# Kernel tuning notes

Hardware: AMD Instinct MI355X
Metric: run time of the kernel (lower is better)

The kernel has to match this reference:

```python
import jax, jax.numpy as jnp
import numpy as np

KS = 5
NF = 64
B, H, W = 2, 160, 160


def _conv1x1(x, w, b):
    # x: (B,Ci,H,W), w: (Co,Ci)
    return jnp.einsum('oi,bihw->bohw', w, x) + b[None, :, None, None]


def _conv2x2(x, w, b, dil):
    # x: (B,1,Hp,Wp), w: (64,1,2,2); VALID conv with dilation dil
    y = jax.lax.conv_general_dilated(x, w, (1, 1), 'VALID',
                                     rhs_dilation=(dil, dil),
                                     dimension_numbers=('NCHW', 'OIHW', 'NCHW'))
    return y + b[None, :, None, None]


def _conv_s(x, w, b):
    # conv1 module, mode 's': gather taps (0,0),(1,1),(1,2),(2,1) of each 3x3 patch,
    # then (1,4) conv == linear combo of 4 shifted images.
    h = x.shape[2] - 2
    wd = x.shape[3] - 2
    x0 = x[:, 0]
    taps = jnp.stack([x0[:, 0:h, 0:wd],
                      x0[:, 1:h + 1, 1:wd + 1],
                      x0[:, 1:h + 1, 2:wd + 2],
                      x0[:, 2:h + 2, 1:wd + 1]], axis=1)  # (B,4,h,wd)
    return jnp.einsum('ok,bkhw->bohw', w.reshape(NF, 4), taps) + b[None, :, None, None]


def _construct(c, dense_ps):
    # relu then dense 1x1-conv chain with channel concat, final 1x1 -> 4 channels
    x = jax.nn.relu(c)
    for (wt, bs) in dense_ps[:-1]:
        feat = jax.nn.relu(_conv1x1(x, wt, bs))
        x = jnp.concatenate([x, feat], axis=1)
    wt, bs = dense_ps[-1]
    return _conv1x1(x, wt, bs)


def _ag(x, sigx, sigy, theta, sigr):
    # x: (B,ks,ks,HW); params: (B,HW). Per-pixel anisotropic bilateral kernel.
    ks = x.shape[1]
    r = jnp.arange(ks, dtype=x.dtype) - ks // 2
    sq = (r[:, None] ** 2 + r[None, :] ** 2)[None, :, :, None]  # (1,ks,ks,1)
    sx = sigx[:, None, None, :]
    sy = sigy[:, None, None, :]
    th = theta[:, None, None, :]
    sr = sigr[:, None, None, :]
    spatial = jnp.exp(-sq / (2.0 * sr ** 2))
    disx = jnp.abs(x[:, ks // 2:ks // 2 + 1] - x)       # center row
    disy = jnp.abs(x[:, :, ks // 2:ks // 2 + 1] - x)    # center col
    a = sx * disx
    bb = sy * disy
    color = jnp.exp(-0.5 * (a ** 2 - 2.0 * th * a * bb + bb ** 2))
    kern = spatial * color
    kern = kern / jnp.sum(kern, axis=(1, 2), keepdims=True)
    return jnp.sum(kern * x, axis=(1, 2))  # (B,HW)


def _forward(x_in, conv1x_w, conv1x_b, conv1c_w, conv1c_b, conv1cs_w, conv1cs_b,
             w2, b2, w3, b3, w4, b4, w5, b5, w6, b6):
    dense_ps = [(w2, b2), (w3, b3), (w4, b4), (w5, b5), (w6, b6)]

    def fk(x, mod):
        if mod == 's':
            c = _conv_s(x, conv1cs_w, conv1cs_b)
        elif mod == 'c':
            c = _conv2x2(x, conv1c_w, conv1c_b, 2)
        else:
            c = _conv2x2(x, conv1x_w, conv1x_b, 1)
        return _construct(c, dense_ps)

    def mode_ens(x, p, mod):
        pad = lambda z: jnp.pad(z, ((0, 0), (0, 0), (0, p), (0, p)), mode='reflect')
        r0 = fk(pad(x), mod)
        r2 = jnp.rot90(fk(pad(jnp.rot90(x, 2, (2, 3))), mod), 2, (2, 3))
        r1 = jnp.rot90(fk(pad(jnp.rot90(x, 1, (2, 3))), mod), 3, (2, 3))
        r3 = jnp.rot90(fk(pad(jnp.rot90(x, 3, (2, 3))), mod), 1, (2, 3))
        return (r0 + r2) / 2.0, (r1 + r3) / 2.0

    e1x, e2x = mode_ens(x_in, 1, 'x')
    e1s, e2s = mode_ens(x_in, 2, 's')
    e1c, e2c = mode_ens(x_in, 2, 'c')
    par = (e1x + e2x + e1s + e2s + e1c + e2c) / 6.0  # (B,4,H,W)

    b, c, h, w = x_in.shape
    sigx = jnp.clip(jax.nn.sigmoid(par[:, 0]).reshape(b, -1) + 1e-6, 0.0, 1.0)
    sigy = jnp.clip(jax.nn.sigmoid(par[:, 1]).reshape(b, -1) + 1e-6, 0.0, 1.0)
    theta = jnp.clip(jnp.tanh(par[:, 2]).reshape(b, -1), -1.0, 1.0)
    sigr = jnp.clip(jnp.tanh(par[:, 3]).reshape(b, -1) + 1e-6, -1.0, 1.0)

    ph = KS // 2
    xt = jnp.pad(x_in, ((0, 0), (0, 0), (ph, ph), (ph, ph)))  # zero pad
    # unfold -> (B, KS, KS, H*W)
    patches = jnp.stack([jnp.stack([xt[:, 0, i:i + h, j:j + w].reshape(b, -1)
                                    for j in range(KS)], axis=1)
                         for i in range(KS)], axis=1)
    outs = _ag(patches, sigx * 20.0, sigy * 20.0, theta, sigr * 10.0 + 10.0).reshape(b, c, h, w)
    return outs, sigx, sigy, theta, sigr


def setup_inputs() -> dict:
    key = jax.random.key(0)
    k = jax.random.split(key, 10)
    def kn(kk, shape, fan_in):
        return jax.random.normal(kk, shape, jnp.float32) * np.float32(np.sqrt(2.0 / fan_in))
    zb = lambda n: jnp.zeros((n,), jnp.float32)
    return {
        'x_in': jax.random.normal(k[0], (B, 1, H, W), jnp.float32),
        'conv1x_w': kn(k[1], (NF, 1, 2, 2), 4), 'conv1x_b': zb(NF),
        'conv1c_w': kn(k[2], (NF, 1, 2, 2), 4), 'conv1c_b': zb(NF),
        'conv1cs_w': kn(k[3], (NF, 1, 1, 4), 4), 'conv1cs_b': zb(NF),
        'w2': kn(k[4], (NF, NF), NF), 'b2': zb(NF),
        'w3': kn(k[5], (NF, 2 * NF), 2 * NF), 'b3': zb(NF),
        'w4': kn(k[6], (NF, 3 * NF), 3 * NF), 'b4': zb(NF),
        'w5': kn(k[7], (NF, 4 * NF), 4 * NF), 'b5': zb(NF),
        'w6': kn(k[8], (4, 5 * NF), 5 * NF), 'b6': zb(4),
    }


def reference(x_in, conv1x_w, conv1x_b, conv1c_w, conv1c_b, conv1cs_w, conv1cs_b,
              w2, b2, w3, b3, w4, b4, w5, b5, w6, b6):
    return _forward(x_in, conv1x_w, conv1x_b, conv1c_w, conv1c_b, conv1cs_w, conv1cs_b,
                    w2, b2, w3, b3, w4, b4, w5, b5, w6, b6)
```

## Files before the change

### kernel.cpp

```cpp
#include <hip/hip_runtime.h>
#include <math.h>


#define NN   160
#define NPIX 25600

typedef __attribute__((ext_vector_type(4))) float float4v;
typedef __attribute__((ext_vector_type(8))) unsigned short ushort8;
typedef __attribute__((ext_vector_type(4))) unsigned short ushort4v;
typedef __attribute__((ext_vector_type(8))) __bf16 bf16x8;

__device__ __forceinline__ int refp(int a) { return (a <= NN - 1) ? a : (2 * (NN - 1) - a); }

__device__ __forceinline__ unsigned short f2b(float f) {
    unsigned int x = __float_as_uint(f);
    return (unsigned short)((x + 0x7FFFu + ((x >> 16) & 1u)) >> 16);
}

__global__ __launch_bounds__(256) void bnet_wconv_kernel(
    const float* __restrict__ w2, const float* __restrict__ w3,
    const float* __restrict__ w4, const float* __restrict__ w5,
    const float* __restrict__ w6, unsigned short* __restrict__ wb)
{
    const int t = blockIdx.x * 256 + threadIdx.x;
    if (t < 4096)       wb[t] = f2b(w2[t]);
    else if (t < 12288) wb[t] = f2b(w3[t - 4096]);
    else if (t < 24576) wb[t] = f2b(w4[t - 12288]);
    else if (t < 40960) wb[t] = f2b(w5[t - 24576]);
    else {
        const int i = t - 40960;
        wb[t] = (i < 4 * 320) ? f2b(w6[i]) : (unsigned short)0;
    }
}

template <int NCH>
__device__ __forceinline__ void dense_layer(const ushort8 (&A)[NCH], float4v biasv,
                                            unsigned short* Xs, int w, int lo16, int lq) {
    const int K = NCH * 32;
#pragma unroll
    for (int pp = 0; pp < 2; ++pp) {
        const int px0 = (pp * 2) * 16 + lo16;
        const int px1 = (pp * 2 + 1) * 16 + lo16;
        float4v acc0 = biasv, acc1 = biasv;
#pragma unroll
        for (int s = 0; s < NCH; ++s) {
            const int c8 = s * 4 + lq;
            const bf16x8 bf0 = __builtin_bit_cast(bf16x8, *(const ushort8*)&Xs[c8 * 512 + px0 * 8]);
            const bf16x8 bf1 = __builtin_bit_cast(bf16x8, *(const ushort8*)&Xs[c8 * 512 + px1 * 8]);
            const bf16x8 af  = __builtin_bit_cast(bf16x8, A[s]);
            acc0 = __builtin_amdgcn_mfma_f32_16x16x32_bf16(af, bf0, acc0, 0, 0, 0);
            acc1 = __builtin_amdgcn_mfma_f32_16x16x32_bf16(af, bf1, acc1, 0, 0, 0);
        }
        const int cb = K + w * 16 + lq * 4;
        ushort4v o0, o1;
#pragma unroll
        for (int r = 0; r < 4; ++r) {
            o0[r] = f2b(fmaxf(acc0[r], 0.0f));
            o1[r] = f2b(fmaxf(acc1[r], 0.0f));
        }
        *(ushort4v*)&Xs[(cb >> 3) * 512 + px0 * 8 + (cb & 7)] = o0;
        *(ushort4v*)&Xs[(cb >> 3) * 512 + px1 * 8 + (cb & 7)] = o1;
    }
    __syncthreads();
}

__global__ __launch_bounds__(256) void bnet_mlp_kernel(
    const float* __restrict__ x,
    const float* __restrict__ wx, const float* __restrict__ bx,
    const float* __restrict__ wcs, const float* __restrict__ bcs,
    const float* __restrict__ wc, const float* __restrict__ bc,
    const unsigned short* __restrict__ wb,
    const float* __restrict__ b2, const float* __restrict__ b3,
    const float* __restrict__ b4, const float* __restrict__ b5,
    const float* __restrict__ b6,
    float* __restrict__ par)
{
    __shared__ unsigned short Xs[20480];
    __shared__ float red[4][4][16][4];

    const int t = threadIdx.x;
    const int lane = t & 63;
    const int lo16 = lane & 15;
    const int lq = lane >> 4;
    const int w = __builtin_amdgcn_readfirstlane(t >> 6);

    const int bid = blockIdx.x;
    const int tg = bid % 200;
    const int b = (bid / 200) & 1;
    const int mode = bid / 400;

    const float* xb = x + b * NPIX;
    const float* w1 = (mode == 0) ? wx : (mode == 1) ? wcs : wc;
    const float* b1 = (mode == 0) ? bx : (mode == 1) ? bcs : bc;
    int DY[4], DX[4];
    if (mode == 0)      { DY[0]=0; DY[1]=0; DY[2]=1; DY[3]=1;  DX[0]=0; DX[1]=1; DX[2]=0; DX[3]=1; }
    else if (mode == 1) { DY[0]=0; DY[1]=1; DY[2]=1; DY[3]=2;  DX[0]=0; DX[1]=1; DX[2]=2; DX[3]=1; }
    else                { DY[0]=0; DY[1]=0; DY[2]=2; DY[3]=2;  DX[0]=0; DX[1]=2; DX[2]=0; DX[3]=2; }

    const int arow = w * 16 + lo16;
    ushort8 a2[2], a3[4], a4[6], a5[8], a6[3];
#pragma unroll
    for (int s = 0; s < 2; ++s) a2[s] = *(const ushort8*)&wb[arow * 64 + s * 32 + lq * 8];
#pragma unroll
    for (int s = 0; s < 4; ++s) a3[s] = *(const ushort8*)&wb[4096 + arow * 128 + s * 32 + lq * 8];
#pragma unroll
    for (int s = 0; s < 6; ++s) a4[s] = *(const ushort8*)&wb[12288 + arow * 192 + s * 32 + lq * 8];
#pragma unroll
    for (int s = 0; s < 8; ++s) a5[s] = *(const ushort8*)&wb[24576 + arow * 256 + s * 32 + lq * 8];
#pragma unroll
    for (int c = 0; c < 3; ++c) {
        const int ch = (3 * w + c) * 32;
        if (ch < 320) {
            a6[c] = *(const ushort8*)&wb[40960 + lo16 * 320 + ch + lq * 8];
        } else {
            ushort8 z = {0, 0, 0, 0, 0, 0, 0, 0};
            a6[c] = z;
        }
    }

    const float4v b2v = *(const float4v*)&b2[w * 16 + lq * 4];
    const float4v b3v = *(const float4v*)&b3[w * 16 + lq * 4];
    const float4v b4v = *(const float4v*)&b4[w * 16 + lq * 4];
    const float4v b5v = *(const float4v*)&b5[w * 16 + lq * 4];

    for (int t2 = 0; t2 < 2; ++t2) {
        const int tile = tg * 2 + t2;
        const int pix = tile * 64 + lane;
        const int pi = pix / NN;
        const int pj = pix - pi * NN;

        float4v acc6[4];
#pragma unroll
        for (int pt = 0; pt < 4; ++pt) { float4v z = {0.f, 0.f, 0.f, 0.f}; acc6[pt] = z; }

        for (int k = 0; k < 4; ++k) {
            __syncthreads();

            float s4[4];
#pragma unroll
            for (int tt = 0; tt < 4; ++tt) {
                const int dy = DY[tt], dx = DX[tt];
                int r, c;
                if (k == 0)      { r = refp(pi + dy); c = refp(pj + dx); }
                else if (k == 1) { r = refp(pi + dx); c = (pj >= dy) ? (pj - dy) : (dy - pj); }
                else if (k == 2) { r = (pi >= dy) ? (pi - dy) : (dy - pi);
                                   c = (pj >= dx) ? (pj - dx) : (dx - pj); }
                else             { r = (pi >= dx) ? (pi - dx) : (dx - pi); c = refp(pj + dy); }
                s4[tt] = xb[r * NN + c];
            }
            ushort8 pk0, pk1;
#pragma unroll
            for (int oo = 0; oo < 16; ++oo) {
                const int o = w * 16 + oo;
                float cacc = b1[o];
#pragma unroll
                for (int tt = 0; tt < 4; ++tt) cacc = fmaf(w1[o * 4 + tt], s4[tt], cacc);
                const unsigned short v = f2b(fmaxf(cacc, 0.0f));
                if (oo < 8) pk0[oo] = v; else pk1[oo - 8] = v;
            }
            *(ushort8*)&Xs[(w * 2) * 512 + lane * 8]     = pk0;
            *(ushort8*)&Xs[(w * 2 + 1) * 512 + lane * 8] = pk1;
            __syncthreads();

            dense_layer<2>(a2, b2v, Xs, w, lo16, lq);
            dense_layer<4>(a3, b3v, Xs, w, lo16, lq);
            dense_layer<6>(a4, b4v, Xs, w, lo16, lq);
            dense_layer<8>(a5, b5v, Xs, w, lo16, lq);

#pragma unroll
            for (int pt = 0; pt < 4; ++pt) {
                const int px = pt * 16 + lo16;
#pragma unroll
                for (int c = 0; c < 3; ++c) {
                    int chb = (3 * w + c) * 32;
                    chb = (chb < 288) ? chb : 288;
                    const int c8 = (chb >> 3) + lq;
                    const bf16x8 bf = __builtin_bit_cast(
                        bf16x8, *(const ushort8*)&Xs[c8 * 512 + px * 8]);
                    const bf16x8 af = __builtin_bit_cast(bf16x8, a6[c]);
                    acc6[pt] = __builtin_amdgcn_mfma_f32_16x16x32_bf16(af, bf, acc6[pt], 0, 0, 0);
                }
            }
        }

        if (lq == 0) {
#pragma unroll
            for (int pt = 0; pt < 4; ++pt)
                *(float4v*)&red[w][pt][lo16][0] = acc6[pt];
        }
        __syncthreads();
        if (w == 0) {
            float4v sv;
#pragma unroll
            for (int r = 0; r < 4; ++r)
                sv[r] = red[0][lq][lo16][r] + red[1][lq][lo16][r]
                      + red[2][lq][lo16][r] + red[3][lq][lo16][r];
            const int pixg = tile * 64 + lq * 16 + lo16;
#pragma unroll
            for (int r = 0; r < 4; ++r)
                atomicAdd(&par[(r * 2 + b) * NPIX + pixg], sv[r] + 4.0f * b6[r]);
        }
    }
}

__global__ __launch_bounds__(256) void bnet_bilateral_kernel(
    const float* __restrict__ x, float* __restrict__ out)
{
    const int tid = blockIdx.x * 256 + threadIdx.x;
    const int b = tid / NPIX;
    const int pix = tid - b * NPIX;
    const int pi = pix / NN;
    const int pj = pix - pi * NN;

    float* par = out + 2 * NPIX;
    const float inv12 = 1.0f / 12.0f;
    const float p0 = par[(0 + b) * NPIX + pix] * inv12;
    const float p1 = par[(2 + b) * NPIX + pix] * inv12;
    const float p2 = par[(4 + b) * NPIX + pix] * inv12;
    const float p3 = par[(6 + b) * NPIX + pix] * inv12;

    float sigx = 1.0f / (1.0f + expf(-p0)) + 1e-6f;
    sigx = fminf(fmaxf(sigx, 0.0f), 1.0f);
    float sigy = 1.0f / (1.0f + expf(-p1)) + 1e-6f;
    sigy = fminf(fmaxf(sigy, 0.0f), 1.0f);
    float th = tanhf(p2);
    th = fminf(fmaxf(th, -1.0f), 1.0f);
    float sigr = tanhf(p3) + 1e-6f;
    sigr = fminf(fmaxf(sigr, -1.0f), 1.0f);

    par[(0 + b) * NPIX + pix] = sigx;
    par[(2 + b) * NPIX + pix] = sigy;
    par[(4 + b) * NPIX + pix] = th;
    par[(6 + b) * NPIX + pix] = sigr;

    const float sx = sigx * 20.0f;
    const float sy = sigy * 20.0f;
    const float sr = sigr * 10.0f + 10.0f;

    const float* xb = x + b * NPIX;
    float patch[5][5];
#pragma unroll
    for (int ky = 0; ky < 5; ++ky) {
#pragma unroll
        for (int kx = 0; kx < 5; ++kx) {
            const int r = pi + ky - 2, c = pj + kx - 2;
            patch[ky][kx] = (r >= 0 && r < NN && c >= 0 && c < NN) ? xb[r * NN + c] : 0.0f;
        }
    }

    const float inv2sr2 = 1.0f / (2.0f * sr * sr);
    float num = 0.0f, den = 0.0f;
#pragma unroll
    for (int ky = 0; ky < 5; ++ky) {
#pragma unroll
        for (int kx = 0; kx < 5; ++kx) {
            const float v = patch[ky][kx];
            const float dxv = fabsf(patch[2][kx] - v);
            const float dyv = fabsf(patch[ky][2] - v);
            const float a = sx * dxv;
            const float bb = sy * dyv;
            const float sq = (float)((ky - 2) * (ky - 2) + (kx - 2) * (kx - 2));
            const float kern = expf(-sq * inv2sr2 - 0.5f * (a * a - 2.0f * th * a * bb + bb * bb));
            den += kern;
            num = fmaf(kern, v, num);
        }
    }
    out[tid] = num / den;
}

extern "C" void kernel_launch(void* const* d_in, const int* in_sizes, int n_in,
                              void* d_out, int out_size, void* d_ws, size_t ws_size,
                              hipStream_t stream) {
    const float* x   = (const float*)d_in[0];
    const float* wx  = (const float*)d_in[1];
    const float* bx  = (const float*)d_in[2];
    const float* wc  = (const float*)d_in[3];
    const float* bc  = (const float*)d_in[4];
    const float* wcs = (const float*)d_in[5];
    const float* bcs = (const float*)d_in[6];
    const float* w2  = (const float*)d_in[7];
    const float* b2  = (const float*)d_in[8];
    const float* w3  = (const float*)d_in[9];
    const float* b3  = (const float*)d_in[10];
    const float* w4  = (const float*)d_in[11];
    const float* b4  = (const float*)d_in[12];
    const float* w5  = (const float*)d_in[13];
    const float* b5  = (const float*)d_in[14];
    const float* w6  = (const float*)d_in[15];
    const float* b6  = (const float*)d_in[16];
    float* out = (float*)d_out;
    unsigned short* wb = (unsigned short*)d_ws;

    hipMemsetAsync(out + 2 * NPIX, 0, 8 * NPIX * sizeof(float), stream);

    hipLaunchKernelGGL(bnet_wconv_kernel, dim3(180), dim3(256), 0, stream,
                       w2, w3, w4, w5, w6, wb);

    hipLaunchKernelGGL(bnet_mlp_kernel, dim3(1200), dim3(256), 0, stream,
                       x, wx, bx, wcs, bcs, wc, bc,
                       wb, b2, b3, b4, b5, b6,
                       out + 2 * NPIX);

    hipLaunchKernelGGL(bnet_bilateral_kernel, dim3(200), dim3(256), 0, stream,
                       x, out);
}
```

Baseline: 193.4 us.

## Split MLP work per rotation across more blocks and use packed bf16 conversion

The MLP kernel used to loop over two tiles and four rotations inside each of 1200 blocks. Each block now handles a single tile and rotation, giving 9600 blocks with launch bounds set for higher occupancy. The reduction buffer now aliases the activation shared memory, and the final bias is folded into the bilateral kernel instead of being added per atomic. Float-to-bf16 packing uses the paired conversion intrinsic, and the bilateral kernel switches to fast __expf with a hand-written tanh. The cost is that every block reloads its weight fragments from global memory, atomics onto the parameter buffer increase fourfold, and the fast exp and tanh lose some accuracy.

```diff
diff --git a/kernel.cpp b/kernel.cpp
--- a/kernel.cpp
+++ b/kernel.cpp
@@ -1,5 +1,7 @@
 #include <hip/hip_runtime.h>
+#include <hip/hip_bf16.h>
 #include <math.h>
+#include <string.h>
 
 
 #define NN   160
@@ -7,7 +9,8 @@
 
 typedef __attribute__((ext_vector_type(4))) float float4v;
 typedef __attribute__((ext_vector_type(8))) unsigned short ushort8;
-typedef __attribute__((ext_vector_type(4))) unsigned short ushort4v;
+typedef __attribute__((ext_vector_type(2))) unsigned int uint2v;
+typedef __attribute__((ext_vector_type(4))) unsigned int uint4v;
 typedef __attribute__((ext_vector_type(8))) __bf16 bf16x8;
 
 __device__ __forceinline__ int refp(int a) { return (a <= NN - 1) ? a : (2 * (NN - 1) - a); }
@@ -15,6 +18,13 @@
 __device__ __forceinline__ unsigned short f2b(float f) {
     unsigned int x = __float_as_uint(f);
     return (unsigned short)((x + 0x7FFFu + ((x >> 16) & 1u)) >> 16);
+}
+__device__ __forceinline__ unsigned int pk2(float lo, float hi) {
+    float2 f; f.x = lo; f.y = hi;
+    __hip_bfloat162 h = __float22bfloat162_rn(f);
+    unsigned int u;
+    memcpy(&u, &h, 4);
+    return u;
 }
 
 __global__ __launch_bounds__(256) void bnet_wconv_kernel(
@@ -52,19 +62,18 @@
             acc1 = __builtin_amdgcn_mfma_f32_16x16x32_bf16(af, bf1, acc1, 0, 0, 0);
         }
         const int cb = K + w * 16 + lq * 4;
-        ushort4v o0, o1;
-#pragma unroll
-        for (int r = 0; r < 4; ++r) {
-            o0[r] = f2b(fmaxf(acc0[r], 0.0f));
-            o1[r] = f2b(fmaxf(acc1[r], 0.0f));
-        }
-        *(ushort4v*)&Xs[(cb >> 3) * 512 + px0 * 8 + (cb & 7)] = o0;
-        *(ushort4v*)&Xs[(cb >> 3) * 512 + px1 * 8 + (cb & 7)] = o1;
+        uint2v o0, o1;
+        o0[0] = pk2(fmaxf(acc0[0], 0.0f), fmaxf(acc0[1], 0.0f));
+        o0[1] = pk2(fmaxf(acc0[2], 0.0f), fmaxf(acc0[3], 0.0f));
+        o1[0] = pk2(fmaxf(acc1[0], 0.0f), fmaxf(acc1[1], 0.0f));
+        o1[1] = pk2(fmaxf(acc1[2], 0.0f), fmaxf(acc1[3], 0.0f));
+        *(uint2v*)&Xs[(cb >> 3) * 512 + px0 * 8 + (cb & 7)] = o0;
+        *(uint2v*)&Xs[(cb >> 3) * 512 + px1 * 8 + (cb & 7)] = o1;
     }
     __syncthreads();
 }
 
-__global__ __launch_bounds__(256) void bnet_mlp_kernel(
+__global__ __launch_bounds__(256, 4) void bnet_mlp_kernel(
     const float* __restrict__ x,
     const float* __restrict__ wx, const float* __restrict__ bx,
     const float* __restrict__ wcs, const float* __restrict__ bcs,
@@ -72,11 +81,10 @@
     const unsigned short* __restrict__ wb,
     const float* __restrict__ b2, const float* __restrict__ b3,
     const float* __restrict__ b4, const float* __restrict__ b5,
-    const float* __restrict__ b6,
     float* __restrict__ par)
 {
     __shared__ unsigned short Xs[20480];
-    __shared__ float red[4][4][16][4];
+    float* red = (float*)Xs;
 
     const int t = threadIdx.x;
     const int lane = t & 63;
@@ -85,9 +93,10 @@
     const int w = __builtin_amdgcn_readfirstlane(t >> 6);
 
     const int bid = blockIdx.x;
-    const int tg = bid % 200;
-    const int b = (bid / 200) & 1;
-    const int mode = bid / 400;
+    const int tile = bid % 400;
+    const int b = (bid / 400) & 1;
+    const int mode = (bid / 800) % 3;
+    const int k = bid / 2400;
 
     const float* xb = x + b * NPIX;
     const float* w1 = (mode == 0) ? wx : (mode == 1) ? wcs : wc;
@@ -117,94 +126,94 @@
             a6[c] = z;
         }
     }
-
     const float4v b2v = *(const float4v*)&b2[w * 16 + lq * 4];
     const float4v b3v = *(const float4v*)&b3[w * 16 + lq * 4];
     const float4v b4v = *(const float4v*)&b4[w * 16 + lq * 4];
     const float4v b5v = *(const float4v*)&b5[w * 16 + lq * 4];
 
-    for (int t2 = 0; t2 < 2; ++t2) {
-        const int tile = tg * 2 + t2;
-        const int pix = tile * 64 + lane;
-        const int pi = pix / NN;
-        const int pj = pix - pi * NN;
-
-        float4v acc6[4];
-#pragma unroll
-        for (int pt = 0; pt < 4; ++pt) { float4v z = {0.f, 0.f, 0.f, 0.f}; acc6[pt] = z; }
-
-        for (int k = 0; k < 4; ++k) {
-            __syncthreads();
-
-            float s4[4];
-#pragma unroll
-            for (int tt = 0; tt < 4; ++tt) {
-                const int dy = DY[tt], dx = DX[tt];
-                int r, c;
-                if (k == 0)      { r = refp(pi + dy); c = refp(pj + dx); }
-                else if (k == 1) { r = refp(pi + dx); c = (pj >= dy) ? (pj - dy) : (dy - pj); }
-                else if (k == 2) { r = (pi >= dy) ? (pi - dy) : (dy - pi);
-                                   c = (pj >= dx) ? (pj - dx) : (dx - pj); }
-                else             { r = (pi >= dx) ? (pi - dx) : (dx - pi); c = refp(pj + dy); }
-                s4[tt] = xb[r * NN + c];
-            }
-            ushort8 pk0, pk1;
-#pragma unroll
-            for (int oo = 0; oo < 16; ++oo) {
-                const int o = w * 16 + oo;
-                float cacc = b1[o];
-#pragma unroll
-                for (int tt = 0; tt < 4; ++tt) cacc = fmaf(w1[o * 4 + tt], s4[tt], cacc);
-                const unsigned short v = f2b(fmaxf(cacc, 0.0f));
-                if (oo < 8) pk0[oo] = v; else pk1[oo - 8] = v;
-            }
-            *(ushort8*)&Xs[(w * 2) * 512 + lane * 8]     = pk0;
-            *(ushort8*)&Xs[(w * 2 + 1) * 512 + lane * 8] = pk1;
-            __syncthreads();
-
-            dense_layer<2>(a2, b2v, Xs, w, lo16, lq);
-            dense_layer<4>(a3, b3v, Xs, w, lo16, lq);
-            dense_layer<6>(a4, b4v, Xs, w, lo16, lq);
-            dense_layer<8>(a5, b5v, Xs, w, lo16, lq);
-
-#pragma unroll
-            for (int pt = 0; pt < 4; ++pt) {
-                const int px = pt * 16 + lo16;
-#pragma unroll
-                for (int c = 0; c < 3; ++c) {
-                    int chb = (3 * w + c) * 32;
-                    chb = (chb < 288) ? chb : 288;
-                    const int c8 = (chb >> 3) + lq;
-                    const bf16x8 bf = __builtin_bit_cast(
-                        bf16x8, *(const ushort8*)&Xs[c8 * 512 + px * 8]);
-                    const bf16x8 af = __builtin_bit_cast(bf16x8, a6[c]);
-                    acc6[pt] = __builtin_amdgcn_mfma_f32_16x16x32_bf16(af, bf, acc6[pt], 0, 0, 0);
-                }
-            }
-        }
-
-        if (lq == 0) {
-#pragma unroll
-            for (int pt = 0; pt < 4; ++pt)
-                *(float4v*)&red[w][pt][lo16][0] = acc6[pt];
-        }
-        __syncthreads();
-        if (w == 0) {
-            float4v sv;
-#pragma unroll
-            for (int r = 0; r < 4; ++r)
-                sv[r] = red[0][lq][lo16][r] + red[1][lq][lo16][r]
-                      + red[2][lq][lo16][r] + red[3][lq][lo16][r];
-            const int pixg = tile * 64 + lq * 16 + lo16;
-#pragma unroll
-            for (int r = 0; r < 4; ++r)
-                atomicAdd(&par[(r * 2 + b) * NPIX + pixg], sv[r] + 4.0f * b6[r]);
-        }
+    const int pix = tile * 64 + lane;
+    const int pi = pix / NN;
+    const int pj = pix - pi * NN;
+
+    float s4[4];
+#pragma unroll
+    for (int tt = 0; tt < 4; ++tt) {
+        const int dy = DY[tt], dx = DX[tt];
+        int r, c;
+        if (k == 0)      { r = refp(pi + dy); c = refp(pj + dx); }
+        else if (k == 1) { r = refp(pi + dx); c = (pj >= dy) ? (pj - dy) : (dy - pj); }
+        else if (k == 2) { r = (pi >= dy) ? (pi - dy) : (dy - pi);
+                           c = (pj >= dx) ? (pj - dx) : (dx - pj); }
+        else             { r = (pi >= dx) ? (pi - dx) : (dx - pi); c = refp(pj + dy); }
+        s4[tt] = xb[r * NN + c];
+    }
+    float co[16];
+#pragma unroll
+    for (int oo = 0; oo < 16; ++oo) {
+        const int o = w * 16 + oo;
+        float cacc = b1[o];
+#pragma unroll
+        for (int tt = 0; tt < 4; ++tt) cacc = fmaf(w1[o * 4 + tt], s4[tt], cacc);
+        co[oo] = fmaxf(cacc, 0.0f);
+    }
+    uint4v pka, pkb;
+#pragma unroll
+    for (int q = 0; q < 4; ++q) {
+        pka[q] = pk2(co[2 * q], co[2 * q + 1]);
+        pkb[q] = pk2(co[8 + 2 * q], co[9 + 2 * q]);
+    }
+    *(uint4v*)&Xs[(w * 2) * 512 + lane * 8]     = pka;
+    *(uint4v*)&Xs[(w * 2 + 1) * 512 + lane * 8] = pkb;
+    __syncthreads();
+
+    dense_layer<2>(a2, b2v, Xs, w, lo16, lq);
+    dense_layer<4>(a3, b3v, Xs, w, lo16, lq);
+    dense_layer<6>(a4, b4v, Xs, w, lo16, lq);
+    dense_layer<8>(a5, b5v, Xs, w, lo16, lq);
+
+    float4v acc6[4];
+#pragma unroll
+    for (int pt = 0; pt < 4; ++pt) { float4v z = {0.f, 0.f, 0.f, 0.f}; acc6[pt] = z; }
+#pragma unroll
+    for (int pt = 0; pt < 4; ++pt) {
+        const int px = pt * 16 + lo16;
+#pragma unroll
+        for (int c = 0; c < 3; ++c) {
+            int chb = (3 * w + c) * 32;
+            chb = (chb < 288) ? chb : 288;
+            const int c8 = (chb >> 3) + lq;
+            const bf16x8 bf = __builtin_bit_cast(
+                bf16x8, *(const ushort8*)&Xs[c8 * 512 + px * 8]);
+            const bf16x8 af = __builtin_bit_cast(bf16x8, a6[c]);
+            acc6[pt] = __builtin_amdgcn_mfma_f32_16x16x32_bf16(af, bf, acc6[pt], 0, 0, 0);
+        }
+    }
+    __syncthreads();
+
+    if (lq == 0) {
+#pragma unroll
+        for (int pt = 0; pt < 4; ++pt)
+            *(float4v*)&red[(((w * 4) + pt) * 16 + lo16) * 4] = acc6[pt];
+    }
+    __syncthreads();
+    if (w == 0) {
+        float4v sv;
+#pragma unroll
+        for (int r = 0; r < 4; ++r)
+            sv[r] = red[(((0 * 4) + lq) * 16 + lo16) * 4 + r]
+                  + red[(((1 * 4) + lq) * 16 + lo16) * 4 + r]
+                  + red[(((2 * 4) + lq) * 16 + lo16) * 4 + r]
+                  + red[(((3 * 4) + lq) * 16 + lo16) * 4 + r];
+        const int pixg = tile * 64 + lq * 16 + lo16;
+#pragma unroll
+        for (int r = 0; r < 4; ++r)
+            atomicAdd(&par[(r * 2 + b) * NPIX + pixg], sv[r]);
     }
 }
 
 __global__ __launch_bounds__(256) void bnet_bilateral_kernel(
-    const float* __restrict__ x, float* __restrict__ out)
+    const float* __restrict__ x, const float* __restrict__ b6,
+    float* __restrict__ out)
 {
     const int tid = blockIdx.x * 256 + threadIdx.x;
     const int b = tid / NPIX;
@@ -214,18 +223,20 @@
 
     float* par = out + 2 * NPIX;
     const float inv12 = 1.0f / 12.0f;
-    const float p0 = par[(0 + b) * NPIX + pix] * inv12;
-    const float p1 = par[(2 + b) * NPIX + pix] * inv12;
-    const float p2 = par[(4 + b) * NPIX + pix] * inv12;
-    const float p3 = par[(6 + b) * NPIX + pix] * inv12;
-
-    float sigx = 1.0f / (1.0f + expf(-p0)) + 1e-6f;
+    const float p0 = par[(0 + b) * NPIX + pix] * inv12 + b6[0];
+    const float p1 = par[(2 + b) * NPIX + pix] * inv12 + b6[1];
+    const float p2 = par[(4 + b) * NPIX + pix] * inv12 + b6[2];
+    const float p3 = par[(6 + b) * NPIX + pix] * inv12 + b6[3];
+
+    float sigx = 1.0f / (1.0f + __expf(-p0)) + 1e-6f;
     sigx = fminf(fmaxf(sigx, 0.0f), 1.0f);
-    float sigy = 1.0f / (1.0f + expf(-p1)) + 1e-6f;
+    float sigy = 1.0f / (1.0f + __expf(-p1)) + 1e-6f;
     sigy = fminf(fmaxf(sigy, 0.0f), 1.0f);
-    float th = tanhf(p2);
+    float t2 = __expf(2.0f * fminf(fmaxf(p2, -15.0f), 15.0f));
+    float th = (t2 - 1.0f) / (t2 + 1.0f);
     th = fminf(fmaxf(th, -1.0f), 1.0f);
-    float sigr = tanhf(p3) + 1e-6f;
+    float t3 = __expf(2.0f * fminf(fmaxf(p3, -15.0f), 15.0f));
+    float sigr = (t3 - 1.0f) / (t3 + 1.0f) + 1e-6f;
     sigr = fminf(fmaxf(sigr, -1.0f), 1.0f);
 
     par[(0 + b) * NPIX + pix] = sigx;
@@ -260,7 +271,7 @@
             const float a = sx * dxv;
             const float bb = sy * dyv;
             const float sq = (float)((ky - 2) * (ky - 2) + (kx - 2) * (kx - 2));
-            const float kern = expf(-sq * inv2sr2 - 0.5f * (a * a - 2.0f * th * a * bb + bb * bb));
+            const float kern = __expf(-sq * inv2sr2 - 0.5f * (a * a - 2.0f * th * a * bb + bb * bb));
             den += kern;
             num = fmaf(kern, v, num);
         }
@@ -291,16 +302,16 @@
     float* out = (float*)d_out;
     unsigned short* wb = (unsigned short*)d_ws;
 
-    hipMemsetAsync(out + 2 * NPIX, 0, 8 * NPIX * sizeof(float), stream);
+    (void)hipMemsetAsync(out + 2 * NPIX, 0, 8 * NPIX * sizeof(float), stream);
 
     hipLaunchKernelGGL(bnet_wconv_kernel, dim3(180), dim3(256), 0, stream,
                        w2, w3, w4, w5, w6, wb);
 
-    hipLaunchKernelGGL(bnet_mlp_kernel, dim3(1200), dim3(256), 0, stream,
+    hipLaunchKernelGGL(bnet_mlp_kernel, dim3(9600), dim3(256), 0, stream,
                        x, wx, bx, wcs, bcs, wc, bc,
-                       wb, b2, b3, b4, b5, b6,
+                       wb, b2, b3, b4, b5,
                        out + 2 * NPIX);
 
     hipLaunchKernelGGL(bnet_bilateral_kernel, dim3(200), dim3(256), 0, stream,
-                       x, out);
-}
+                       x, b6, out);
+}
```

New measurement: 198.9 us. 2.9% more time.
